# Kernel optimization log

Hardware: AMD Instinct MI355X
Metric: run time of the kernel (lower is better)

## Reference

```python
import jax, jax.numpy as jnp
import numpy as np

FREQ = 16          # matches init kwarg 'freq'
TWO_PI = 2.0 * np.pi

def _square(phase):
    # scipy.signal.square with duty=0.5: +1 where (phase mod 2*pi) < pi, else -1
    return jnp.where(jnp.mod(phase, TWO_PI) < np.pi, 1.0, -1.0).astype(jnp.float32)

def setup_inputs() -> dict:
    key = jax.random.key(0)
    x = jax.random.uniform(key, (4194304, 1), dtype=jnp.float32)
    return {"x": x}

def reference(x):
    # torch loop: for i in range(freq-1): x = cat([x, square(2*pi*t*2**i)], -1)
    N, D = x.shape
    f = (2.0 ** jnp.arange(FREQ - 1)).astype(jnp.float32)        # [F-1]
    phase = TWO_PI * x[:, None, :] * f[None, :, None]            # [N, F-1, D]
    sq = _square(phase).reshape(N, (FREQ - 1) * D)               # block order matches cat
    return jnp.concatenate([x, sq], axis=-1)                     # [N, D*FREQ]
```

## Files before the change

kernel.cpp:

```cpp
#include <hip/hip_runtime.h>
#include <stdint.h>


__global__ __launch_bounds__(256) void encoder_kernel(
    const float* __restrict__ x, float* __restrict__ out, int nthreads)
{
    int t = blockIdx.x * 256 + threadIdx.x;
    if (t >= nthreads) return;
    int n = t >> 2;
    int qpart = t & 3;

    float xv = x[n];
    float tv = 6.28318530717958647692f * xv;

    uint32_t bits = __float_as_uint(tv);
    int E = (int)(bits >> 23) - 127;
    uint32_t mant = (bits & 0x7FFFFFu) | 0x800000u;

    constexpr uint32_t M = 13176795u;
    constexpr uint64_t G = 0xFFFFFFFFFFFFFFFFull / M + 1ull;
    uint64_t q = __umul64hi(((uint64_t)mant) << 15, G);

    int base = 16 - E;

    float vals[4];
    int c0 = qpart << 2;
    #pragma unroll
    for (int k = 0; k < 4; ++k) {
        int c = c0 + k;
        float v;
        if (c == 0) {
            v = xv;
        } else {
            int s = base - (c - 1);
            uint32_t bit = (s >= 0 && s < 64) ? (uint32_t)((q >> s) & 1ull) : 0u;
            v = bit ? -1.0f : 1.0f;
        }
        vals[k] = v;
    }
    float4 res;
    res.x = vals[0]; res.y = vals[1]; res.z = vals[2]; res.w = vals[3];
    reinterpret_cast<float4*>(out)[t] = res;
}

extern "C" void kernel_launch(void* const* d_in, const int* in_sizes, int n_in,
                              void* d_out, int out_size, void* d_ws, size_t ws_size,
                              hipStream_t stream) {
    const float* x = (const float*)d_in[0];
    float* out = (float*)d_out;
    int nrows = in_sizes[0];
    int nthreads = nrows * 4;
    int blocks = (nthreads + 255) / 256;
    encoder_kernel<<<blocks, 256, 0, stream>>>(x, out, nthreads);
}
```

Before: 290.4 us.

## Process several float4 chunks per thread with nontemporal stores and branchless sign bits

Each thread now handles eight strided output quarters instead of one, which cuts the block count. Output goes through nontemporal vector stores so the 256 MB write stream bypasses cache retention. The square-wave sign is built by OR-ing a shifted bit into the float encoding of 1.0, using a 32-bit quotient with the shift clamped. The risk is that clamping the shift to 31 could give wrong bits for shifts at or beyond 32, where the old code produced zero.

```diff
diff --git a/kernel.cpp b/kernel.cpp
--- a/kernel.cpp
+++ b/kernel.cpp
@@ -2,45 +2,54 @@
 #include <stdint.h>
 
 
+typedef float v4f __attribute__((ext_vector_type(4)));
+
+constexpr int ITER = 8;
+
 __global__ __launch_bounds__(256) void encoder_kernel(
-    const float* __restrict__ x, float* __restrict__ out, int nthreads)
+    const float* __restrict__ x, float* __restrict__ out, int nquarters)
 {
-    int t = blockIdx.x * 256 + threadIdx.x;
-    if (t >= nthreads) return;
-    int n = t >> 2;
-    int qpart = t & 3;
-
-    float xv = x[n];
-    float tv = 6.28318530717958647692f * xv;
-
-    uint32_t bits = __float_as_uint(tv);
-    int E = (int)(bits >> 23) - 127;
-    uint32_t mant = (bits & 0x7FFFFFu) | 0x800000u;
+    const int T = gridDim.x * 256;
+    const int t0 = blockIdx.x * 256 + threadIdx.x;
 
     constexpr uint32_t M = 13176795u;
     constexpr uint64_t G = 0xFFFFFFFFFFFFFFFFull / M + 1ull;
-    uint64_t q = __umul64hi(((uint64_t)mant) << 15, G);
 
-    int base = 16 - E;
+    #pragma unroll
+    for (int j = 0; j < ITER; ++j) {
+        int idx = t0 + j * T;
+        if (idx >= nquarters) continue;
+        int n = idx >> 2;
+        int qpart = idx & 3;
 
-    float vals[4];
-    int c0 = qpart << 2;
-    #pragma unroll
-    for (int k = 0; k < 4; ++k) {
-        int c = c0 + k;
-        float v;
-        if (c == 0) {
-            v = xv;
-        } else {
-            int s = base - (c - 1);
-            uint32_t bit = (s >= 0 && s < 64) ? (uint32_t)((q >> s) & 1ull) : 0u;
-            v = bit ? -1.0f : 1.0f;
+        float xv = x[n];
+        float tv = 6.28318530717958647692f * xv;
+
+        uint32_t bits = __float_as_uint(tv);
+        int E = (int)(bits >> 23) - 127;
+        uint32_t mant = (bits & 0x7FFFFFu) | 0x800000u;
+
+        uint32_t q = (uint32_t)__umul64hi(((uint64_t)mant) << 15, G);
+        int base = 16 - E;
+
+        int c0 = qpart << 2;
+        v4f res;
+        #pragma unroll
+        for (int k = 0; k < 4; ++k) {
+            int c = c0 + k;
+            float v;
+            if (c == 0) {
+                v = xv;
+            } else {
+                uint32_t s = (uint32_t)(base - (c - 1));
+                s = s > 31u ? 31u : s;
+                uint32_t bit = (q >> s) & 1u;
+                v = __uint_as_float(0x3F800000u | (bit << 31));
+            }
+            res[k] = v;
         }
-        vals[k] = v;
+        __builtin_nontemporal_store(res, reinterpret_cast<v4f*>(out) + idx);
     }
-    float4 res;
-    res.x = vals[0]; res.y = vals[1]; res.z = vals[2]; res.w = vals[3];
-    reinterpret_cast<float4*>(out)[t] = res;
 }
 
 extern "C" void kernel_launch(void* const* d_in, const int* in_sizes, int n_in,
@@ -49,7 +58,8 @@
     const float* x = (const float*)d_in[0];
     float* out = (float*)d_out;
     int nrows = in_sizes[0];
-    int nthreads = nrows * 4;
-    int blocks = (nthreads + 255) / 256;
-    encoder_kernel<<<blocks, 256, 0, stream>>>(x, out, nthreads);
+    int nquarters = nrows * 4;
+    int threads_needed = (nquarters + ITER - 1) / ITER;
+    int blocks = (threads_needed + 255) / 256;
+    encoder_kernel<<<blocks, 256, 0, stream>>>(x, out, nquarters);
 }
```

Measured after the change: 277.5 us. -4.5%, faster.
